# Performance work log

Hardware: AMD Instinct MI355X
Metric: run time of the kernel (lower is better)

## Reference

```python
import jax, jax.numpy as jnp
import numpy as np

B, D, C = 4096, 256, 64  # batch, dim_embed, n_conditions
EPS = 1e-10


def setup_inputs() -> dict:
    key = jax.random.key(0)
    k1, k2, k3, k4 = jax.random.split(key, 4)
    x = jax.random.normal(k1, (B, D), dtype=jnp.float32)          # embedded_x (embeddingnet = identity)
    W = jax.random.normal(k2, (C, D, D), dtype=jnp.float32) * 0.02  # per-condition Linear weights (out,in)
    b = jax.random.normal(k3, (C, D), dtype=jnp.float32) * 0.02     # per-condition Linear biases
    c = jax.random.randint(k4, (B,), 0, C)                         # condition index per sample
    return {"x": x, "W": W, "b": b, "c": c}


def reference(x, W, b, c):
    # per-sample expert Linear: y_i = W[c_i] @ x_i + b[c_i]
    y = jnp.einsum('bij,bj->bi', W[c], x) + b[c]          # [B, D]
    # mask_norm accumulates L1 norm of the selected weight PER SAMPLE (duplicates counted)
    per_cond_l1 = jnp.sum(jnp.abs(W), axis=(1, 2))        # [C]
    mask_norm = jnp.sum(per_cond_l1[c])
    # embed_norm = global L2 (Frobenius) norm of embedded_x
    embed_norm = jnp.sqrt(jnp.sum(x * x))
    # F.normalize(p=2, dim=1, eps=1e-10): divide by max(row_norm, eps)
    row_norm = jnp.sqrt(jnp.sum(y * y, axis=1, keepdims=True))
    masked_embedding = y / jnp.maximum(row_norm, EPS)
    return (masked_embedding, mask_norm, embed_norm, x)
```

## Files before the change

kernel.cpp:

```cpp
#include <hip/hip_runtime.h>
#include <math.h>

#define B_ 4096
#define D_ 256
#define C_ 64
#define BD (B_*D_)

typedef __attribute__((ext_vector_type(8))) short bf16x8;
typedef __attribute__((ext_vector_type(4))) float f32x4;

__device__ __forceinline__ float wave_reduce_sum(float v) {
    #pragma unroll
    for (int off = 1; off < 64; off <<= 1) v += __shfl_xor(v, off);
    return v;
}

__device__ __forceinline__ unsigned cvtpk(float lo, float hi) {
    unsigned r;
    asm volatile("v_cvt_pk_bf16_f32 %0, %1, %2" : "=v"(r) : "v"(lo), "v"(hi));
    return r;
}

__global__ __launch_bounds__(256, 4) void k_main(const float* __restrict__ W,
                                                 const float* __restrict__ b,
                                                 const float* __restrict__ x,
                                                 const int* __restrict__ c,
                                                 float* __restrict__ out,
                                                 float* __restrict__ l1p,
                                                 float* __restrict__ xsqp,
                                                 int* __restrict__ cnt4) {
    int hw = blockIdx.x;
    int bid = (hw & 7) * 128 + (hw >> 3);
    int cond = bid >> 4;
    int ct = (bid >> 2) & 3;
    int sl = bid & 3;
    int tid = threadIdx.x;
    int wv = tid >> 6, lane = tid & 63;
    int g = lane >> 4, fr = lane & 15;

    const float4* x4 = (const float4*)x;
    int xi = bid * 256 + tid;
    float4 xv = x4[xi];
    int4 cvq[4];
    #pragma unroll
    for (int t = 0; t < 4; ++t) cvq[t] = ((const int4*)c)[t * 256 + tid];
    const float4* Wp = (const float4*)(W + (size_t)cond * 65536 + (size_t)(ct * 64 + wv * 16 + fr) * 256) + g * 2;
    float4 w0a = Wp[0], w0b = Wp[1];
    float4 w1a = Wp[8], w1b = Wp[9];
    float bias_s = b[cond * 256 + ct * 64 + wv * 16 + fr];

    __shared__ unsigned Xl[48 * 128];
    __shared__ float part_x[4];
    __shared__ float part_w[4];
    __shared__ int slist[48];
    __shared__ int nlist;
    if (tid == 0) nlist = 0;

    float2* dst = (float2*)(out + BD + 2);
    dst[2 * xi]     = make_float2(xv.x, xv.y);
    dst[2 * xi + 1] = make_float2(xv.z, xv.w);
    float s = xv.x * xv.x + xv.y * xv.y + xv.z * xv.z + xv.w * xv.w;
    s = wave_reduce_sum(s);
    if (lane == 0) part_x[wv] = s;
    __syncthreads();

    #pragma unroll
    for (int t = 0; t < 4; ++t) {
        int4 q = cvq[t];
        int cc = (sl == 0) ? q.x : (sl == 1) ? q.y : (sl == 2) ? q.z : q.w;
        if (cc == cond) {
            int p = atomicAdd(&nlist, 1);
            if (p < 48) slist[p] = 4 * (t * 256 + tid) + sl;
        }
    }
    __syncthreads();
    int n = min(nlist, 48);
    int mts = (n + 15) >> 4;
    if (tid == 0) {
        xsqp[bid] = (part_x[0] + part_x[1]) + (part_x[2] + part_x[3]);
        if (ct == 0) cnt4[cond * 4 + sl] = n;
    }

    int sgr[12];
    #pragma unroll
    for (int k = 0; k < 12; ++k) sgr[k] = slist[wv + 4 * k];
    #pragma unroll
    for (int k = 0; k < 12; ++k) {
        int u = tid + 256 * k;
        if (u < n * 64) {
            int si = u >> 6, v = u & 63;
            float4 q = x4[(size_t)sgr[k] * 64 + v];
            int off = (v * 8) ^ ((si & 7) << 4);
            Xl[si * 128 + (off >> 2)]     = cvtpk(q.x, q.y);
            Xl[si * 128 + (off >> 2) + 1] = cvtpk(q.z, q.w);
        }
    }
    __syncthreads();

    f32x4 acc[3];
    #pragma unroll
    for (int mt = 0; mt < 3; ++mt) acc[mt] = (f32x4){0.f, 0.f, 0.f, 0.f};
    float l1acc = 0.f;

    #pragma unroll
    for (int kk = 0; kk < 8; ++kk) {
        bf16x8 bfr;
        unsigned* bp = (unsigned*)&bfr;
        bp[0] = cvtpk(w0a.x, w0a.y); bp[1] = cvtpk(w0a.z, w0a.w);
        bp[2] = cvtpk(w0b.x, w0b.y); bp[3] = cvtpk(w0b.z, w0b.w);
        if (sl == 0)
            l1acc += fabsf(w0a.x) + fabsf(w0a.y) + fabsf(w0a.z) + fabsf(w0a.w)
                   + fabsf(w0b.x) + fabsf(w0b.y) + fabsf(w0b.z) + fabsf(w0b.w);
        #pragma unroll
        for (int mt = 0; mt < 3; ++mt) if (mt < mts) {
            int row = mt * 16 + fr;
            bf16x8 afr = *(const bf16x8*)((const char*)Xl + row * 512 + ((kk * 64 + g * 16) ^ ((row & 7) << 4)));
            acc[mt] = __builtin_amdgcn_mfma_f32_16x16x32_bf16(afr, bfr, acc[mt], 0, 0, 0);
        }
        w0a = w1a; w0b = w1b;
        if (kk < 6) { w1a = Wp[(kk + 2) * 8]; w1b = Wp[(kk + 2) * 8 + 1]; }
    }

    if (sl == 0) {
        float a = wave_reduce_sum(l1acc);
        if (lane == 0) part_w[wv] = a;
    }
    __syncthreads();
    if (sl == 0 && tid == 0)
        l1p[cond * 4 + ct] = (part_w[0] + part_w[1]) + (part_w[2] + part_w[3]);

    #pragma unroll
    for (int mt = 0; mt < 3; ++mt) if (mt < mts) {
        #pragma unroll
        for (int j = 0; j < 4; ++j) {
            int row = mt * 16 + g * 4 + j;
            if (row < n) {
                int sg = slist[row];
                out[(size_t)sg * 256 + ct * 64 + wv * 16 + fr] = acc[mt][j] + bias_s;
            }
        }
    }
}

__global__ __launch_bounds__(256) void k_fin(float* __restrict__ out,
                                             const float* __restrict__ xsqp,
                                             const float* __restrict__ l1p,
                                             const int* __restrict__ cnt4) {
    int tid = threadIdx.x;
    int wv = tid >> 6, lane = tid & 63;
    if (blockIdx.x == 1024) {
        __shared__ float part[4];
        float s = 0.f;
        #pragma unroll
        for (int j = 0; j < 4; ++j) s += xsqp[tid * 4 + j];
        s = wave_reduce_sum(s);
        if (lane == 0) part[wv] = s;
        __syncthreads();
        if (tid < 64) {
            float l1 = (l1p[tid * 4 + 0] + l1p[tid * 4 + 1]) + (l1p[tid * 4 + 2] + l1p[tid * 4 + 3]);
            float cnt = (float)((cnt4[tid * 4 + 0] + cnt4[tid * 4 + 1]) + (cnt4[tid * 4 + 2] + cnt4[tid * 4 + 3]));
            float mv = l1 * cnt;
            mv = wave_reduce_sum(mv);
            if (tid == 0) out[BD] = mv;
        }
        if (tid == 0) out[BD + 1] = sqrtf((part[0] + part[1]) + (part[2] + part[3]));
        return;
    }
    int rowv = blockIdx.x * 4 + wv;
    float4* p = (float4*)out + (size_t)rowv * 64 + lane;
    float4 v = *p;
    float s = v.x * v.x + v.y * v.y + v.z * v.z + v.w * v.w;
    s = wave_reduce_sum(s);
    float inv = 1.0f / fmaxf(sqrtf(s), 1e-10f);
    v.x *= inv; v.y *= inv; v.z *= inv; v.w *= inv;
    *p = v;
}

extern "C" void kernel_launch(void* const* d_in, const int* in_sizes, int n_in,
                              void* d_out, int out_size, void* d_ws, size_t ws_size,
                              hipStream_t stream) {
    const float* x = (const float*)d_in[0];
    const float* W = (const float*)d_in[1];
    const float* b = (const float*)d_in[2];
    const int*   c = (const int*)d_in[3];
    float* out = (float*)d_out;

    float* xsqp = (float*)d_ws;
    float* l1p  = xsqp + 1024;
    int*   cnt4 = (int*)(l1p + 256);

    k_main<<<1024, 256, 0, stream>>>(W, b, x, c, out, l1p, xsqp, cnt4);
    k_fin<<<1025, 256, 0, stream>>>(out, xsqp, l1p, cnt4);
}
```

Baseline: 21.11 us.

## Halve k_main grid and stage bf16 W tile in LDS via coalesced loads

Each block now covers half of a condition's samples (up to 64 rows) instead of a quarter, so the grid shrinks from 1024 to 512 blocks and every W tile is loaded and converted half as often. W is read with a row-contiguous coalesced pattern, converted once to bf16 and stored in padded LDS, and MFMA B fragments are read from LDS instead of strided global loads. The cost is more LDS per block, 16 float4 registers held for W, a fixed 64-row cap per block, and lower parallelism with only 512 blocks.

Result: slower. 25.97 us (+23.0%).

```diff
diff --git a/kernel.cpp b/kernel.cpp
--- a/kernel.cpp
+++ b/kernel.cpp
@@ -21,104 +21,118 @@
     return r;
 }
 
-__global__ __launch_bounds__(256, 4) void k_main(const float* __restrict__ W,
+__global__ __launch_bounds__(256, 2) void k_main(const float* __restrict__ W,
                                                  const float* __restrict__ b,
                                                  const float* __restrict__ x,
                                                  const int* __restrict__ c,
                                                  float* __restrict__ out,
                                                  float* __restrict__ l1p,
                                                  float* __restrict__ xsqp,
-                                                 int* __restrict__ cnt4) {
+                                                 int* __restrict__ cnt2) {
     int hw = blockIdx.x;
-    int bid = (hw & 7) * 128 + (hw >> 3);
-    int cond = bid >> 4;
-    int ct = (bid >> 2) & 3;
-    int sl = bid & 3;
+    int bid = (hw & 7) * 64 + (hw >> 3);
+    int cond = bid >> 3;
+    int ct = (bid >> 1) & 3;
+    int sl = bid & 1;
     int tid = threadIdx.x;
     int wv = tid >> 6, lane = tid & 63;
     int g = lane >> 4, fr = lane & 15;
+    int r = tid >> 2, q = tid & 3;
 
     const float4* x4 = (const float4*)x;
-    int xi = bid * 256 + tid;
-    float4 xv = x4[xi];
-    int4 cvq[4];
-    #pragma unroll
-    for (int t = 0; t < 4; ++t) cvq[t] = ((const int4*)c)[t * 256 + tid];
-    const float4* Wp = (const float4*)(W + (size_t)cond * 65536 + (size_t)(ct * 64 + wv * 16 + fr) * 256) + g * 2;
-    float4 w0a = Wp[0], w0b = Wp[1];
-    float4 w1a = Wp[8], w1b = Wp[9];
+    int xi = bid * 512 + tid;
+    float4 xv0 = x4[xi];
+    float4 xv1 = x4[xi + 256];
+    const int4* c4 = (const int4*)c;
+    int4 cq[4];
+    cq[0] = c4[2 * tid];     cq[1] = c4[2 * tid + 1];
+    cq[2] = c4[2 * tid + 512]; cq[3] = c4[2 * tid + 513];
+    const float4* Wt4 = (const float4*)(W + (size_t)cond * 65536) + (size_t)(ct * 64 + r) * 64 + q * 16;
+    float4 wr[16];
+    #pragma unroll
+    for (int j = 0; j < 16; ++j) wr[j] = Wt4[j];
     float bias_s = b[cond * 256 + ct * 64 + wv * 16 + fr];
 
-    __shared__ unsigned Xl[48 * 128];
+    __shared__ unsigned Xl[64 * 128];
+    __shared__ unsigned Wf[64 * 132];
     __shared__ float part_x[4];
     __shared__ float part_w[4];
-    __shared__ int slist[48];
+    __shared__ int slist[64];
     __shared__ int nlist;
     if (tid == 0) nlist = 0;
 
     float2* dst = (float2*)(out + BD + 2);
-    dst[2 * xi]     = make_float2(xv.x, xv.y);
-    dst[2 * xi + 1] = make_float2(xv.z, xv.w);
-    float s = xv.x * xv.x + xv.y * xv.y + xv.z * xv.z + xv.w * xv.w;
+    dst[2 * xi]             = make_float2(xv0.x, xv0.y);
+    dst[2 * xi + 1]         = make_float2(xv0.z, xv0.w);
+    dst[2 * (xi + 256)]     = make_float2(xv1.x, xv1.y);
+    dst[2 * (xi + 256) + 1] = make_float2(xv1.z, xv1.w);
+    float s = xv0.x * xv0.x + xv0.y * xv0.y + xv0.z * xv0.z + xv0.w * xv0.w
+            + xv1.x * xv1.x + xv1.y * xv1.y + xv1.z * xv1.z + xv1.w * xv1.w;
     s = wave_reduce_sum(s);
     if (lane == 0) part_x[wv] = s;
     __syncthreads();
 
     #pragma unroll
     for (int t = 0; t < 4; ++t) {
-        int4 q = cvq[t];
-        int cc = (sl == 0) ? q.x : (sl == 1) ? q.y : (sl == 2) ? q.z : q.w;
-        if (cc == cond) {
-            int p = atomicAdd(&nlist, 1);
-            if (p < 48) slist[p] = 4 * (t * 256 + tid) + sl;
-        }
-    }
-    __syncthreads();
-    int n = min(nlist, 48);
+        int s0 = (t < 2) ? (8 * tid + 4 * t) : (2048 + 8 * tid + 4 * (t - 2));
+        int a  = sl ? cq[t].y : cq[t].x;
+        int b2 = sl ? cq[t].w : cq[t].z;
+        if (a == cond)  { int p = atomicAdd(&nlist, 1); if (p < 64) slist[p] = s0 + sl; }
+        if (b2 == cond) { int p = atomicAdd(&nlist, 1); if (p < 64) slist[p] = s0 + 2 + sl; }
+    }
+    __syncthreads();
+    int n = min(nlist, 64);
     int mts = (n + 15) >> 4;
     if (tid == 0) {
         xsqp[bid] = (part_x[0] + part_x[1]) + (part_x[2] + part_x[3]);
-        if (ct == 0) cnt4[cond * 4 + sl] = n;
-    }
-
-    int sgr[12];
-    #pragma unroll
-    for (int k = 0; k < 12; ++k) sgr[k] = slist[wv + 4 * k];
-    #pragma unroll
-    for (int k = 0; k < 12; ++k) {
+        if (ct == 0) cnt2[cond * 2 + sl] = n;
+    }
+
+    int sgr[16];
+    #pragma unroll
+    for (int k = 0; k < 16; ++k) sgr[k] = slist[wv + 4 * k];
+    #pragma unroll
+    for (int k = 0; k < 16; ++k) {
         int u = tid + 256 * k;
         if (u < n * 64) {
             int si = u >> 6, v = u & 63;
-            float4 q = x4[(size_t)sgr[k] * 64 + v];
+            float4 qv = x4[(size_t)sgr[k] * 64 + v];
             int off = (v * 8) ^ ((si & 7) << 4);
-            Xl[si * 128 + (off >> 2)]     = cvtpk(q.x, q.y);
-            Xl[si * 128 + (off >> 2) + 1] = cvtpk(q.z, q.w);
-        }
-    }
-    __syncthreads();
-
-    f32x4 acc[3];
-    #pragma unroll
-    for (int mt = 0; mt < 3; ++mt) acc[mt] = (f32x4){0.f, 0.f, 0.f, 0.f};
+            uint2 pk = make_uint2(cvtpk(qv.x, qv.y), cvtpk(qv.z, qv.w));
+            *(uint2*)(Xl + si * 128 + (off >> 2)) = pk;
+        }
+    }
+
     float l1acc = 0.f;
+    #pragma unroll
+    for (int jj = 0; jj < 8; ++jj) {
+        uint4 pk;
+        pk.x = cvtpk(wr[2*jj].x,   wr[2*jj].y);
+        pk.y = cvtpk(wr[2*jj].z,   wr[2*jj].w);
+        pk.z = cvtpk(wr[2*jj+1].x, wr[2*jj+1].y);
+        pk.w = cvtpk(wr[2*jj+1].z, wr[2*jj+1].w);
+        *(uint4*)(&Wf[r * 132 + q * 32 + jj * 4]) = pk;
+    }
+    if (sl == 0) {
+        #pragma unroll
+        for (int j = 0; j < 16; ++j)
+            l1acc += fabsf(wr[j].x) + fabsf(wr[j].y) + fabsf(wr[j].z) + fabsf(wr[j].w);
+    }
+    __syncthreads();
+
+    f32x4 acc[4];
+    #pragma unroll
+    for (int mt = 0; mt < 4; ++mt) acc[mt] = (f32x4){0.f, 0.f, 0.f, 0.f};
 
     #pragma unroll
     for (int kk = 0; kk < 8; ++kk) {
-        bf16x8 bfr;
-        unsigned* bp = (unsigned*)&bfr;
-        bp[0] = cvtpk(w0a.x, w0a.y); bp[1] = cvtpk(w0a.z, w0a.w);
-        bp[2] = cvtpk(w0b.x, w0b.y); bp[3] = cvtpk(w0b.z, w0b.w);
-        if (sl == 0)
-            l1acc += fabsf(w0a.x) + fabsf(w0a.y) + fabsf(w0a.z) + fabsf(w0a.w)
-                   + fabsf(w0b.x) + fabsf(w0b.y) + fabsf(w0b.z) + fabsf(w0b.w);
+        bf16x8 bfr = *(const bf16x8*)(Wf + (wv * 16 + fr) * 132 + kk * 32 + g * 4);
         #pragma unroll
-        for (int mt = 0; mt < 3; ++mt) if (mt < mts) {
+        for (int mt = 0; mt < 4; ++mt) if (mt < mts) {
             int row = mt * 16 + fr;
             bf16x8 afr = *(const bf16x8*)((const char*)Xl + row * 512 + ((kk * 64 + g * 16) ^ ((row & 7) << 4)));
             acc[mt] = __builtin_amdgcn_mfma_f32_16x16x32_bf16(afr, bfr, acc[mt], 0, 0, 0);
         }
-        w0a = w1a; w0b = w1b;
-        if (kk < 6) { w1a = Wp[(kk + 2) * 8]; w1b = Wp[(kk + 2) * 8 + 1]; }
     }
 
     if (sl == 0) {
@@ -130,7 +144,7 @@
         l1p[cond * 4 + ct] = (part_w[0] + part_w[1]) + (part_w[2] + part_w[3]);
 
     #pragma unroll
-    for (int mt = 0; mt < 3; ++mt) if (mt < mts) {
+    for (int mt = 0; mt < 4; ++mt) if (mt < mts) {
         #pragma unroll
         for (int j = 0; j < 4; ++j) {
             int row = mt * 16 + g * 4 + j;
@@ -145,20 +159,18 @@
 __global__ __launch_bounds__(256) void k_fin(float* __restrict__ out,
                                              const float* __restrict__ xsqp,
                                              const float* __restrict__ l1p,
-                                             const int* __restrict__ cnt4) {
+                                             const int* __restrict__ cnt2) {
     int tid = threadIdx.x;
     int wv = tid >> 6, lane = tid & 63;
     if (blockIdx.x == 1024) {
         __shared__ float part[4];
-        float s = 0.f;
-        #pragma unroll
-        for (int j = 0; j < 4; ++j) s += xsqp[tid * 4 + j];
+        float s = xsqp[tid] + xsqp[tid + 256];
         s = wave_reduce_sum(s);
         if (lane == 0) part[wv] = s;
         __syncthreads();
         if (tid < 64) {
             float l1 = (l1p[tid * 4 + 0] + l1p[tid * 4 + 1]) + (l1p[tid * 4 + 2] + l1p[tid * 4 + 3]);
-            float cnt = (float)((cnt4[tid * 4 + 0] + cnt4[tid * 4 + 1]) + (cnt4[tid * 4 + 2] + cnt4[tid * 4 + 3]));
+            float cnt = (float)(cnt2[tid * 2] + cnt2[tid * 2 + 1]);
             float mv = l1 * cnt;
             mv = wave_reduce_sum(mv);
             if (tid == 0) out[BD] = mv;
@@ -186,9 +198,9 @@
     float* out = (float*)d_out;
 
     float* xsqp = (float*)d_ws;
-    float* l1p  = xsqp + 1024;
-    int*   cnt4 = (int*)(l1p + 256);
-
-    k_main<<<1024, 256, 0, stream>>>(W, b, x, c, out, l1p, xsqp, cnt4);
-    k_fin<<<1025, 256, 0, stream>>>(out, xsqp, l1p, cnt4);
-}
+    float* l1p  = xsqp + 512;
+    int*   cnt2 = (int*)(l1p + 256);
+
+    k_main<<<512, 256, 0, stream>>>(W, b, x, c, out, l1p, xsqp, cnt2);
+    k_fin<<<1025, 256, 0, stream>>>(out, xsqp, l1p, cnt2);
+}
```

## Split samples into two slices and stage W tiles through double-buffered LDS

Applied to the files above, without the earlier changes.

Each block now covers half of a condition's samples (up to 64 rows) and a 32-column slice of the output, instead of a quarter of the samples and 64 columns. W is loaded with coalesced row-contiguous reads, converted to bf16 and staged in a double-buffered LDS tile shared by the waves, and the waves split the work into row halves and column halves. This cuts redundant W reads per sample-slice and makes the W loads coalesced, at the cost of a __syncthreads per k-step and more LDS per block. The capacity limit rises from 48 to 64 samples per slice, and the partial L1 and count bookkeeping is resized to match.

Measured after the change: 18.76 us. -11.1%, faster.

```diff
diff --git a/kernel.cpp b/kernel.cpp
--- a/kernel.cpp
+++ b/kernel.cpp
@@ -28,15 +28,17 @@
                                                  float* __restrict__ out,
                                                  float* __restrict__ l1p,
                                                  float* __restrict__ xsqp,
-                                                 int* __restrict__ cnt4) {
+                                                 int* __restrict__ cnt2) {
     int hw = blockIdx.x;
     int bid = (hw & 7) * 128 + (hw >> 3);
     int cond = bid >> 4;
-    int ct = (bid >> 2) & 3;
-    int sl = bid & 3;
+    int ct = (bid >> 1) & 7;
+    int sl = bid & 1;
     int tid = threadIdx.x;
     int wv = tid >> 6, lane = tid & 63;
     int g = lane >> 4, fr = lane & 15;
+    int cw = wv & 1, rh = wv >> 1;
+    int r = tid >> 3, ch = tid & 7;
 
     const float4* x4 = (const float4*)x;
     int xi = bid * 256 + tid;
@@ -44,15 +46,16 @@
     int4 cvq[4];
     #pragma unroll
     for (int t = 0; t < 4; ++t) cvq[t] = ((const int4*)c)[t * 256 + tid];
-    const float4* Wp = (const float4*)(W + (size_t)cond * 65536 + (size_t)(ct * 64 + wv * 16 + fr) * 256) + g * 2;
-    float4 w0a = Wp[0], w0b = Wp[1];
-    float4 w1a = Wp[8], w1b = Wp[9];
-    float bias_s = b[cond * 256 + ct * 64 + wv * 16 + fr];
-
-    __shared__ unsigned Xl[48 * 128];
+    const float4* Wt4 = (const float4*)(W + (size_t)cond * 65536) + (size_t)(ct * 32 + r) * 64 + ch;
+    float4 wA = Wt4[0];
+    float4 wB = Wt4[8];
+    float bias_s = b[cond * 256 + ct * 32 + cw * 16 + fr];
+
+    __shared__ unsigned Xl[64 * 128];
+    __shared__ unsigned Wl[2][32 * 20];
     __shared__ float part_x[4];
     __shared__ float part_w[4];
-    __shared__ int slist[48];
+    __shared__ int slist[64];
     __shared__ int nlist;
     if (tid == 0) nlist = 0;
 
@@ -67,58 +70,69 @@
     #pragma unroll
     for (int t = 0; t < 4; ++t) {
         int4 q = cvq[t];
-        int cc = (sl == 0) ? q.x : (sl == 1) ? q.y : (sl == 2) ? q.z : q.w;
-        if (cc == cond) {
-            int p = atomicAdd(&nlist, 1);
-            if (p < 48) slist[p] = 4 * (t * 256 + tid) + sl;
-        }
-    }
-    __syncthreads();
-    int n = min(nlist, 48);
+        int base = 4 * (t * 256 + tid);
+        int a  = sl ? q.y : q.x;
+        int b2 = sl ? q.w : q.z;
+        if (a == cond)  { int p = atomicAdd(&nlist, 1); if (p < 64) slist[p] = base + sl; }
+        if (b2 == cond) { int p = atomicAdd(&nlist, 1); if (p < 64) slist[p] = base + 2 + sl; }
+    }
+    __syncthreads();
+    int n = min(nlist, 64);
     int mts = (n + 15) >> 4;
     if (tid == 0) {
         xsqp[bid] = (part_x[0] + part_x[1]) + (part_x[2] + part_x[3]);
-        if (ct == 0) cnt4[cond * 4 + sl] = n;
-    }
-
-    int sgr[12];
-    #pragma unroll
-    for (int k = 0; k < 12; ++k) sgr[k] = slist[wv + 4 * k];
-    #pragma unroll
-    for (int k = 0; k < 12; ++k) {
+        if (ct == 0) cnt2[cond * 2 + sl] = n;
+    }
+
+    int sgr[16];
+    #pragma unroll
+    for (int k = 0; k < 16; ++k) sgr[k] = slist[wv + 4 * k];
+    #pragma unroll
+    for (int k = 0; k < 16; ++k) {
         int u = tid + 256 * k;
         if (u < n * 64) {
             int si = u >> 6, v = u & 63;
-            float4 q = x4[(size_t)sgr[k] * 64 + v];
+            float4 qv = x4[(size_t)sgr[k] * 64 + v];
             int off = (v * 8) ^ ((si & 7) << 4);
-            Xl[si * 128 + (off >> 2)]     = cvtpk(q.x, q.y);
-            Xl[si * 128 + (off >> 2) + 1] = cvtpk(q.z, q.w);
-        }
-    }
-    __syncthreads();
-
-    f32x4 acc[3];
-    #pragma unroll
-    for (int mt = 0; mt < 3; ++mt) acc[mt] = (f32x4){0.f, 0.f, 0.f, 0.f};
+            uint2 pk = make_uint2(cvtpk(qv.x, qv.y), cvtpk(qv.z, qv.w));
+            *(uint2*)(Xl + si * 128 + (off >> 2)) = pk;
+        }
+    }
+
     float l1acc = 0.f;
+    {
+        uint2 pk = make_uint2(cvtpk(wA.x, wA.y), cvtpk(wA.z, wA.w));
+        *(uint2*)(&Wl[0][r * 20 + ch * 2]) = pk;
+        if (sl == 0)
+            l1acc += fabsf(wA.x) + fabsf(wA.y) + fabsf(wA.z) + fabsf(wA.w);
+    }
+    __syncthreads();
+
+    f32x4 acc[2];
+    acc[0] = (f32x4){0.f, 0.f, 0.f, 0.f};
+    acc[1] = (f32x4){0.f, 0.f, 0.f, 0.f};
 
     #pragma unroll
     for (int kk = 0; kk < 8; ++kk) {
-        bf16x8 bfr;
-        unsigned* bp = (unsigned*)&bfr;
-        bp[0] = cvtpk(w0a.x, w0a.y); bp[1] = cvtpk(w0a.z, w0a.w);
-        bp[2] = cvtpk(w0b.x, w0b.y); bp[3] = cvtpk(w0b.z, w0b.w);
-        if (sl == 0)
-            l1acc += fabsf(w0a.x) + fabsf(w0a.y) + fabsf(w0a.z) + fabsf(w0a.w)
-                   + fabsf(w0b.x) + fabsf(w0b.y) + fabsf(w0b.z) + fabsf(w0b.w);
+        bf16x8 bfr = *(const bf16x8*)(&Wl[kk & 1][(cw * 16 + fr) * 20 + g * 4]);
         #pragma unroll
-        for (int mt = 0; mt < 3; ++mt) if (mt < mts) {
-            int row = mt * 16 + fr;
+        for (int mt = 0; mt < 2; ++mt) if (rh * 2 + mt < mts) {
+            int row = rh * 32 + mt * 16 + fr;
             bf16x8 afr = *(const bf16x8*)((const char*)Xl + row * 512 + ((kk * 64 + g * 16) ^ ((row & 7) << 4)));
             acc[mt] = __builtin_amdgcn_mfma_f32_16x16x32_bf16(afr, bfr, acc[mt], 0, 0, 0);
         }
-        w0a = w1a; w0b = w1b;
-        if (kk < 6) { w1a = Wp[(kk + 2) * 8]; w1b = Wp[(kk + 2) * 8 + 1]; }
+        if (kk < 7) {
+            float4 wsrc = (kk & 1) ? wA : wB;
+            uint2 pk = make_uint2(cvtpk(wsrc.x, wsrc.y), cvtpk(wsrc.z, wsrc.w));
+            *(uint2*)(&Wl[(kk + 1) & 1][r * 20 + ch * 2]) = pk;
+            if (sl == 0)
+                l1acc += fabsf(wsrc.x) + fabsf(wsrc.y) + fabsf(wsrc.z) + fabsf(wsrc.w);
+            if (kk < 6) {
+                if (kk & 1) wB = Wt4[(kk + 2) * 8];
+                else        wA = Wt4[(kk + 2) * 8];
+            }
+            __syncthreads();
+        }
     }
 
     if (sl == 0) {
@@ -127,16 +141,16 @@
     }
     __syncthreads();
     if (sl == 0 && tid == 0)
-        l1p[cond * 4 + ct] = (part_w[0] + part_w[1]) + (part_w[2] + part_w[3]);
-
-    #pragma unroll
-    for (int mt = 0; mt < 3; ++mt) if (mt < mts) {
+        l1p[cond * 8 + ct] = (part_w[0] + part_w[1]) + (part_w[2] + part_w[3]);
+
+    #pragma unroll
+    for (int mt = 0; mt < 2; ++mt) if (rh * 2 + mt < mts) {
         #pragma unroll
         for (int j = 0; j < 4; ++j) {
-            int row = mt * 16 + g * 4 + j;
+            int row = rh * 32 + mt * 16 + g * 4 + j;
             if (row < n) {
                 int sg = slist[row];
-                out[(size_t)sg * 256 + ct * 64 + wv * 16 + fr] = acc[mt][j] + bias_s;
+                out[(size_t)sg * 256 + ct * 32 + cw * 16 + fr] = acc[mt][j] + bias_s;
             }
         }
     }
@@ -145,7 +159,7 @@
 __global__ __launch_bounds__(256) void k_fin(float* __restrict__ out,
                                              const float* __restrict__ xsqp,
                                              const float* __restrict__ l1p,
-                                             const int* __restrict__ cnt4) {
+                                             const int* __restrict__ cnt2) {
     int tid = threadIdx.x;
     int wv = tid >> 6, lane = tid & 63;
     if (blockIdx.x == 1024) {
@@ -157,8 +171,10 @@
         if (lane == 0) part[wv] = s;
         __syncthreads();
         if (tid < 64) {
-            float l1 = (l1p[tid * 4 + 0] + l1p[tid * 4 + 1]) + (l1p[tid * 4 + 2] + l1p[tid * 4 + 3]);
-            float cnt = (float)((cnt4[tid * 4 + 0] + cnt4[tid * 4 + 1]) + (cnt4[tid * 4 + 2] + cnt4[tid * 4 + 3]));
+            float l1 = 0.f;
+            #pragma unroll
+            for (int j = 0; j < 8; ++j) l1 += l1p[tid * 8 + j];
+            float cnt = (float)(cnt2[tid * 2] + cnt2[tid * 2 + 1]);
             float mv = l1 * cnt;
             mv = wave_reduce_sum(mv);
             if (tid == 0) out[BD] = mv;
@@ -187,8 +203,8 @@
 
     float* xsqp = (float*)d_ws;
     float* l1p  = xsqp + 1024;
-    int*   cnt4 = (int*)(l1p + 256);
-
-    k_main<<<1024, 256, 0, stream>>>(W, b, x, c, out, l1p, xsqp, cnt4);
-    k_fin<<<1025, 256, 0, stream>>>(out, xsqp, l1p, cnt4);
-}
+    int*   cnt2 = (int*)(l1p + 512);
+
+    k_main<<<1024, 256, 0, stream>>>(W, b, x, c, out, l1p, xsqp, cnt2);
+    k_fin<<<1025, 256, 0, stream>>>(out, xsqp, l1p, cnt2);
+}
```
